# Kernel optimization log

Hardware: AMD Instinct MI355X
Metric: run time of the kernel (lower is better)

The kernel has to match this reference:

```python
import jax, jax.numpy as jnp
import numpy as np
import math

EMB, HEADS, LATENT, FFN = 1024, 16, 256, 4096
HEAD_DIM = EMB // HEADS
B, N = 2, 2048
EPS = 1e-5


def _layer_norm(x, g, b):
    m = jnp.mean(x, axis=-1, keepdims=True)
    v = jnp.mean(jnp.square(x - m), axis=-1, keepdims=True)
    return (x - m) * jax.lax.rsqrt(v + EPS) * g + b


def setup_inputs() -> dict:
    key = jax.random.key(0)
    ks = jax.random.split(key, 20)
    s = 0.02
    def w(k, shape):
        return jax.random.normal(k, shape, dtype=jnp.float32) * s
    return {
        "x": jax.random.normal(ks[0], (B, N, EMB), dtype=jnp.float32),
        "attn_bias": jax.random.normal(ks[1], (N, N), dtype=jnp.float32),
        "Wq_w": w(ks[2], (EMB, EMB)),   "Wq_b": jnp.zeros((EMB,), jnp.float32),
        "WaK_w": w(ks[3], (EMB, LATENT)), "WaK_b": jnp.zeros((LATENT,), jnp.float32),
        "WbK_w": w(ks[4], (LATENT, EMB)), "WbK_b": jnp.zeros((EMB,), jnp.float32),
        "WaV_w": w(ks[5], (EMB, LATENT)), "WaV_b": jnp.zeros((LATENT,), jnp.float32),
        "WbV_w": w(ks[6], (LATENT, EMB)), "WbV_b": jnp.zeros((EMB,), jnp.float32),
        "Wo_w": w(ks[7], (EMB, EMB)),   "Wo_b": jnp.zeros((EMB,), jnp.float32),
        "ffn1_w": w(ks[8], (EMB, FFN)), "ffn1_b": jnp.zeros((FFN,), jnp.float32),
        "ffn2_w": w(ks[9], (FFN, EMB)), "ffn2_b": jnp.zeros((EMB,), jnp.float32),
        "ln1_g": jnp.ones((EMB,), jnp.float32), "ln1_b": jnp.zeros((EMB,), jnp.float32),
        "ln2_g": jnp.ones((EMB,), jnp.float32), "ln2_b": jnp.zeros((EMB,), jnp.float32),
    }


def reference(x, attn_bias, Wq_w, Wq_b, WaK_w, WaK_b, WbK_w, WbK_b,
              WaV_w, WaV_b, WbV_w, WbV_b, Wo_w, Wo_b,
              ffn1_w, ffn1_b, ffn2_w, ffn2_b, ln1_g, ln1_b, ln2_g, ln2_b):
    b, n, _ = x.shape
    Q = x @ Wq_w + Wq_b                                   # [B,N,E]
    K = (x @ WaK_w + WaK_b) @ WbK_w + WbK_b               # low-rank K
    V = (x @ WaV_w + WaV_b) @ WbV_w + WbV_b               # low-rank V
    Qh = Q.reshape(b, n, HEADS, HEAD_DIM)
    Kh = K.reshape(b, n, HEADS, HEAD_DIM)
    Vh = V.reshape(b, n, HEADS, HEAD_DIM)
    scale = 1.0 / math.sqrt(HEAD_DIM)
    scores = jnp.einsum('bnhd,bmhd->bhnm', Qh, Kh) * scale
    scores = scores + attn_bias[None, None, :, :]
    weights = jax.nn.softmax(scores, axis=-1)
    O = jnp.einsum('bhnm,bmhd->bnhd', weights, Vh).reshape(b, n, EMB)
    O = O @ Wo_w + Wo_b
    x1 = _layer_norm(x + O, ln1_g, ln1_b)
    h = jax.nn.gelu(x1 @ ffn1_w + ffn1_b, approximate=False)
    ffn_out = h @ ffn2_w + ffn2_b
    return _layer_norm(x1 + ffn_out, ln2_g, ln2_b)
```

## Files before the change

kernel.cpp:

```cpp
#include <hip/hip_runtime.h>
#include <hip/hip_bf16.h>
#include <math.h>

typedef __attribute__((ext_vector_type(4))) float f32x4;
typedef __attribute__((ext_vector_type(8))) __bf16 bf16x8;
typedef unsigned short u16;

#define L2E 1.44269504088896f

__device__ __forceinline__ u16 f2b(float f) {
  union { float f; unsigned u; } x; x.f = f;
  unsigned r = x.u + 0x7fffu + ((x.u >> 16) & 1u);
  return (u16)(r >> 16);
}

__device__ __forceinline__ void gl_lds16(const void* g, void* l) {
  __builtin_amdgcn_global_load_lds(
      (const __attribute__((address_space(1))) void*)g,
      (__attribute__((address_space(3))) void*)l, 16, 0, 0);
}

template<int EPI>
__global__ __launch_bounds__(256, 3)
void gemm_bt(const u16* __restrict__ A, int lda,
             const u16* __restrict__ Bt,
             const float* __restrict__ bias,
             void* __restrict__ C, int ldc,
             int M, int N, int K)
{
  __shared__ u16 As[128 * 32];
  __shared__ u16 Bs[128 * 32];
  const int t = threadIdx.x;
  const int lane = t & 63;
  const int w = t >> 6;
  const int wr = w >> 1, wc = w & 1;
  const int row0 = blockIdx.y * 128, col0 = blockIdx.x * 128;
  const int r = lane & 15, g = lane >> 4;

  f32x4 acc[4][4];
#pragma unroll
  for (int m = 0; m < 4; ++m)
#pragma unroll
    for (int n = 0; n < 4; ++n) acc[m][n] = (f32x4){0.f, 0.f, 0.f, 0.f};

  const u16* Ag = A + (size_t)(row0 + (t >> 2)) * lda + (t & 3) * 8;
  const u16* Bg = Bt + (size_t)(col0 + (t >> 2)) * K + (t & 3) * 8;
  u16* Asw  = &As[t * 8];
  u16* Asw2 = &As[(t + 256) * 8];
  u16* Bsw  = &Bs[t * 8];
  u16* Bsw2 = &Bs[(t + 256) * 8];
  const size_t a2 = (size_t)64 * lda, bo2 = (size_t)64 * K;

  for (int kt = 0; kt < K; kt += 32) {
    gl_lds16(Ag + kt, Asw);
    gl_lds16(Ag + a2 + kt, Asw2);
    gl_lds16(Bg + kt, Bsw);
    gl_lds16(Bg + bo2 + kt, Bsw2);
    __syncthreads();
    bf16x8 af[4], bfr[4];
#pragma unroll
    for (int m = 0; m < 4; ++m)
      af[m] = *(const bf16x8*)&As[(wr * 64 + m * 16 + r) * 32 + g * 8];
#pragma unroll
    for (int n = 0; n < 4; ++n)
      bfr[n] = *(const bf16x8*)&Bs[(wc * 64 + n * 16 + r) * 32 + g * 8];
#pragma unroll
    for (int m = 0; m < 4; ++m)
#pragma unroll
      for (int n = 0; n < 4; ++n)
        acc[m][n] = __builtin_amdgcn_mfma_f32_16x16x32_bf16(af[m], bfr[n], acc[m][n], 0, 0, 0);
    __syncthreads();
  }

#pragma unroll
  for (int n = 0; n < 4; ++n) {
    const int col = col0 + wc * 64 + n * 16 + r;
    const float bv = bias[col];
#pragma unroll
    for (int m = 0; m < 4; ++m) {
      const int rb = row0 + wr * 64 + m * 16 + g * 4;
      if constexpr (EPI == 3) {
        const int b_ = rb >> 11, nn = rb & 2047;
        const int h_ = col >> 6, d_ = col & 63;
        u16* vp = (u16*)C + ((size_t)((b_ * 16 + h_) * 64 + d_)) * 2048 + nn;
        ushort4 pk;
        pk.x = f2b(acc[m][n][0] + bv);
        pk.y = f2b(acc[m][n][1] + bv);
        pk.z = f2b(acc[m][n][2] + bv);
        pk.w = f2b(acc[m][n][3] + bv);
        *(ushort4*)vp = pk;
      } else {
#pragma unroll
        for (int j = 0; j < 4; ++j) {
          float v = acc[m][n][j] + bv;
          if constexpr (EPI == 1) v = 0.5f * v * (1.0f + erff(v * 0.70710678118654752f));
          const size_t idx = (size_t)(rb + j) * ldc + col;
          if constexpr (EPI == 2) ((float*)C)[idx] = v;
          else ((u16*)C)[idx] = f2b(v);
        }
      }
    }
  }
}

__global__ __launch_bounds__(256, 4)
void attn_kernel(const u16* __restrict__ Qg,
                 const u16* __restrict__ Kg,
                 const u16* __restrict__ Vt,
                 const float* __restrict__ Bf,
                 u16* __restrict__ O)
{
  const int bh = blockIdx.x;
  const int b = bh >> 4, h = bh & 15;
  const int q0 = blockIdx.y * 64;
  const int t = threadIdx.x;
  const int lane = t & 63;
  const int w = t >> 6;
  const int r = lane & 15, g = lane >> 4;

  __shared__ u16 Ks[64 * 64];
  __shared__ u16 Vs[64 * 64];
  __shared__ __bf16 Ps[4][16 * 64];

  bf16x8 qa[2];
  {
    const size_t qrow = (size_t)(b * 2048 + q0 + w * 16 + r);
    const u16* qp = Qg + qrow * 1536 + h * 64 + g * 8;
    qa[0] = *(const bf16x8*)qp;
    qa[1] = *(const bf16x8*)(qp + 32);
#pragma unroll
    for (int dh = 0; dh < 2; ++dh)
#pragma unroll
      for (int i = 0; i < 8; ++i)
        qa[dh][i] = (__bf16)((float)qa[dh][i] * (0.125f * L2E));
  }

  f32x4 Oa[4];
#pragma unroll
  for (int dc = 0; dc < 4; ++dc) Oa[dc] = (f32x4){0.f, 0.f, 0.f, 0.f};
  float lsum[4] = {0.f, 0.f, 0.f, 0.f};

  const int srow = t >> 3;
  const int spos = t & 7;
  const int sseg  = spos ^ (srow & 7);
  const int srow2 = srow + 32;
  const int sseg2 = spos ^ (srow2 & 7);

  const float* bp = Bf + (size_t)(q0 + w * 16 + g * 4) * 2048 + r;

  for (int mt = 0; mt < 32; ++mt) {
    const int m0 = mt * 64;
    gl_lds16(Kg + (size_t)(b * 2048 + m0 + srow)  * 1024 + h * 64 + sseg * 8,  &Ks[t * 8]);
    gl_lds16(Kg + (size_t)(b * 2048 + m0 + srow2) * 1024 + h * 64 + sseg2 * 8, &Ks[(t + 256) * 8]);
    gl_lds16(Vt + (size_t)(bh * 64 + srow)  * 2048 + m0 + sseg * 8,  &Vs[t * 8]);
    gl_lds16(Vt + (size_t)(bh * 64 + srow2) * 2048 + m0 + sseg2 * 8, &Vs[(t + 256) * 8]);

    f32x4 s[4];
#pragma unroll
    for (int mc = 0; mc < 4; ++mc)
#pragma unroll
      for (int j = 0; j < 4; ++j)
        s[mc][j] = bp[(size_t)j * 2048 + m0 + mc * 16] * L2E;

    __syncthreads();

#pragma unroll
    for (int mc = 0; mc < 4; ++mc) {
      const int mrow = mc * 16 + r;
      const bf16x8 kb0 = *(const bf16x8*)&Ks[mrow * 64 + (((0 * 4 + g) ^ (mrow & 7)) * 8)];
      const bf16x8 kb1 = *(const bf16x8*)&Ks[mrow * 64 + (((1 * 4 + g) ^ (mrow & 7)) * 8)];
      s[mc] = __builtin_amdgcn_mfma_f32_16x16x32_bf16(qa[0], kb0, s[mc], 0, 0, 0);
      s[mc] = __builtin_amdgcn_mfma_f32_16x16x32_bf16(qa[1], kb1, s[mc], 0, 0, 0);
    }

    __bf16* pw = (__bf16*)Ps[w];
#pragma unroll
    for (int mc = 0; mc < 4; ++mc) {
      const int mm = mc * 16 + r;
#pragma unroll
      for (int j = 0; j < 4; ++j) {
        const float p = __builtin_amdgcn_exp2f(s[mc][j]);
        lsum[j] += p;
        const int qr = g * 4 + j;
        pw[qr * 64 + (((mm >> 3) ^ (qr & 7)) * 8) + (mm & 7)] = (__bf16)p;
      }
    }

    const bf16x8 pa0 = *(const bf16x8*)&pw[r * 64 + (((0 * 4 + g) ^ (r & 7)) * 8)];
    const bf16x8 pa1 = *(const bf16x8*)&pw[r * 64 + (((1 * 4 + g) ^ (r & 7)) * 8)];
#pragma unroll
    for (int dc = 0; dc < 4; ++dc) {
      const int drow = dc * 16 + r;
      const bf16x8 vb0 = *(const bf16x8*)&Vs[drow * 64 + (((0 * 4 + g) ^ (drow & 7)) * 8)];
      const bf16x8 vb1 = *(const bf16x8*)&Vs[drow * 64 + (((1 * 4 + g) ^ (drow & 7)) * 8)];
      Oa[dc] = __builtin_amdgcn_mfma_f32_16x16x32_bf16(pa0, vb0, Oa[dc], 0, 0, 0);
      Oa[dc] = __builtin_amdgcn_mfma_f32_16x16x32_bf16(pa1, vb1, Oa[dc], 0, 0, 0);
    }
    __syncthreads();
  }

#pragma unroll
  for (int off = 1; off < 16; off <<= 1)
#pragma unroll
    for (int j = 0; j < 4; ++j) lsum[j] += __shfl_xor(lsum[j], off);

  u16* Os = Ks;
#pragma unroll
  for (int j = 0; j < 4; ++j) {
    const float inv = 1.0f / lsum[j];
    const int qr = w * 16 + g * 4 + j;
#pragma unroll
    for (int dc = 0; dc < 4; ++dc)
      Os[qr * 64 + dc * 16 + r] = f2b(Oa[dc][j] * inv);
  }
  __syncthreads();
#pragma unroll
  for (int i = 0; i < 2; ++i) {
    const int tt = t + i * 256;
    const int orow = tt >> 3, oseg = tt & 7;
    const uint4 v = *(const uint4*)&Os[orow * 64 + oseg * 8];
    *(uint4*)&O[(size_t)(b * 2048 + q0 + orow) * 1024 + h * 64 + oseg * 8] = v;
  }
}

__global__ void cvt_f32_bf16(const float* __restrict__ in, u16* __restrict__ out, int n4)
{
  const int i = blockIdx.x * 256 + threadIdx.x;
  if (i >= n4) return;
  const float4 v = ((const float4*)in)[i];
  ushort4 o;
  o.x = f2b(v.x); o.y = f2b(v.y); o.z = f2b(v.z); o.w = f2b(v.w);
  ((ushort4*)out)[i] = o;
}

__global__ __launch_bounds__(256)
void transpose_f32_bf16(const float* __restrict__ in, u16* __restrict__ out, int R, int C)
{
  __shared__ float tile[32][33];
  const int tx = threadIdx.x, ty = threadIdx.y;
  const int c0 = blockIdx.x * 32, r0 = blockIdx.y * 32;
#pragma unroll
  for (int i = 0; i < 4; ++i)
    tile[ty + i * 8][tx] = in[(size_t)(r0 + ty + i * 8) * C + c0 + tx];
  __syncthreads();
#pragma unroll
  for (int i = 0; i < 4; ++i)
    out[(size_t)(c0 + ty + i * 8) * R + r0 + tx] = f2b(tile[tx][ty + i * 8]);
}

__global__ void concat_bias(const float* __restrict__ a, const float* __restrict__ b,
                            const float* __restrict__ c, float* __restrict__ o)
{
  const int i = blockIdx.x * 256 + threadIdx.x;
  if (i < 1024) o[i] = a[i];
  else if (i < 1280) o[i] = b[i - 1024];
  else if (i < 1536) o[i] = c[i - 1280];
}

template<int WB>
__global__ __launch_bounds__(256)
void ln_kernel(const float* __restrict__ xa, const float* __restrict__ xbr,
               const float* __restrict__ gam, const float* __restrict__ bet,
               float* __restrict__ outf, u16* __restrict__ outb)
{
  const int row = blockIdx.x, t = threadIdx.x;
  const float4 a = ((const float4*)(xa + (size_t)row * 1024))[t];
  const float4 c = ((const float4*)(xbr + (size_t)row * 1024))[t];
  const float v0 = a.x + c.x, v1 = a.y + c.y, v2 = a.z + c.z, v3 = a.w + c.w;
  float s = v0 + v1 + v2 + v3;
  float q = v0 * v0 + v1 * v1 + v2 * v2 + v3 * v3;
#pragma unroll
  for (int off = 1; off < 64; off <<= 1) {
    s += __shfl_xor(s, off);
    q += __shfl_xor(q, off);
  }
  __shared__ float ss[4], qs[4];
  const int w = t >> 6, lane = t & 63;
  if (lane == 0) { ss[w] = s; qs[w] = q; }
  __syncthreads();
  const float S = ss[0] + ss[1] + ss[2] + ss[3];
  const float Q = qs[0] + qs[1] + qs[2] + qs[3];
  const float mean = S * (1.0f / 1024.0f);
  const float var = Q * (1.0f / 1024.0f) - mean * mean;
  const float rstd = rsqrtf(var + 1e-5f);
  const float4 gm = ((const float4*)gam)[t];
  const float4 bt = ((const float4*)bet)[t];
  const float o0 = (v0 - mean) * rstd * gm.x + bt.x;
  const float o1 = (v1 - mean) * rstd * gm.y + bt.y;
  const float o2 = (v2 - mean) * rstd * gm.z + bt.z;
  const float o3 = (v3 - mean) * rstd * gm.w + bt.w;
  float4 ov; ov.x = o0; ov.y = o1; ov.z = o2; ov.w = o3;
  ((float4*)(outf + (size_t)row * 1024))[t] = ov;
  if constexpr (WB) {
    ushort4 ob; ob.x = f2b(o0); ob.y = f2b(o1); ob.z = f2b(o2); ob.w = f2b(o3);
    ((ushort4*)(outb + (size_t)row * 1024))[t] = ob;
  }
}

extern "C" void kernel_launch(void* const* d_in, const int* in_sizes, int n_in,
                              void* d_out, int out_size, void* d_ws, size_t ws_size,
                              hipStream_t stream)
{
  const float* x     = (const float*)d_in[0];
  const float* abias = (const float*)d_in[1];
  const float* Wq_w  = (const float*)d_in[2];
  const float* Wq_b  = (const float*)d_in[3];
  const float* WaK_w = (const float*)d_in[4];
  const float* WaK_b = (const float*)d_in[5];
  const float* WbK_w = (const float*)d_in[6];
  const float* WbK_b = (const float*)d_in[7];
  const float* WaV_w = (const float*)d_in[8];
  const float* WaV_b = (const float*)d_in[9];
  const float* WbV_w = (const float*)d_in[10];
  const float* WbV_b = (const float*)d_in[11];
  const float* Wo_w  = (const float*)d_in[12];
  const float* Wo_b  = (const float*)d_in[13];
  const float* f1_w  = (const float*)d_in[14];
  const float* f1_b  = (const float*)d_in[15];
  const float* f2_w  = (const float*)d_in[16];
  const float* f2_b  = (const float*)d_in[17];
  const float* ln1_g = (const float*)d_in[18];
  const float* ln1_b = (const float*)d_in[19];
  const float* ln2_g = (const float*)d_in[20];
  const float* ln2_b = (const float*)d_in[21];

  char* ws = (char*)d_ws;
  u16*   xb    = (u16*)(ws + 0);
  u16*   WB1   = (u16*)(ws + 8388608);
  u16*   WbKT  = (u16*)(ws + 11534336);
  u16*   WbVT  = (u16*)(ws + 12058624);
  u16*   WoT   = (u16*)(ws + 12582912);
  u16*   F1T   = (u16*)(ws + 14680064);
  u16*   F2T   = (u16*)(ws + 23068672);
  float* bias1 = (float*)(ws + 31457280);
  u16*   G1    = (u16*)(ws + 39854080);
  u16*   Kb    = (u16*)(ws + 52436992);
  u16*   Vt    = (u16*)(ws + 60825600);
  u16*   Ob    = (u16*)(ws + 69214208);
  float* Y     = (float*)(ws + 77602816);
  float* x1f   = (float*)(ws + 94380032);
  u16*   x1b   = (u16*)(ws + 111157248);
  u16*   hbuf  = G1;

  cvt_f32_bf16<<<4096, 256, 0, stream>>>(x, xb, 1048576);
  transpose_f32_bf16<<<dim3(32, 32), dim3(32, 8), 0, stream>>>(Wq_w, WB1, 1024, 1024);
  transpose_f32_bf16<<<dim3(8, 32),  dim3(32, 8), 0, stream>>>(WaK_w, WB1 + 1024 * 1024, 1024, 256);
  transpose_f32_bf16<<<dim3(8, 32),  dim3(32, 8), 0, stream>>>(WaV_w, WB1 + 1280 * 1024, 1024, 256);
  transpose_f32_bf16<<<dim3(32, 8),  dim3(32, 8), 0, stream>>>(WbK_w, WbKT, 256, 1024);
  transpose_f32_bf16<<<dim3(32, 8),  dim3(32, 8), 0, stream>>>(WbV_w, WbVT, 256, 1024);
  transpose_f32_bf16<<<dim3(32, 32), dim3(32, 8), 0, stream>>>(Wo_w, WoT, 1024, 1024);
  transpose_f32_bf16<<<dim3(128, 32), dim3(32, 8), 0, stream>>>(f1_w, F1T, 1024, 4096);
  transpose_f32_bf16<<<dim3(32, 128), dim3(32, 8), 0, stream>>>(f2_w, F2T, 4096, 1024);
  concat_bias<<<6, 256, 0, stream>>>(Wq_b, WaK_b, WaV_b, bias1);

  gemm_bt<0><<<dim3(12, 32), 256, 0, stream>>>(xb, 1024, WB1, bias1, G1, 1536, 4096, 1536, 1024);
  gemm_bt<0><<<dim3(8, 32), 256, 0, stream>>>(G1 + 1024, 1536, WbKT, WbK_b, Kb, 1024, 4096, 1024, 256);
  gemm_bt<3><<<dim3(8, 32), 256, 0, stream>>>(G1 + 1280, 1536, WbVT, WbV_b, Vt, 2048, 4096, 1024, 256);
  attn_kernel<<<dim3(32, 32), 256, 0, stream>>>(G1, Kb, Vt, abias, Ob);
  gemm_bt<2><<<dim3(8, 32), 256, 0, stream>>>(Ob, 1024, WoT, Wo_b, Y, 1024, 4096, 1024, 1024);
  ln_kernel<1><<<4096, 256, 0, stream>>>(x, Y, ln1_g, ln1_b, x1f, x1b);
  gemm_bt<1><<<dim3(32, 32), 256, 0, stream>>>(x1b, 1024, F1T, f1_b, hbuf, 4096, 4096, 4096, 1024);
  gemm_bt<2><<<dim3(8, 32), 256, 0, stream>>>(hbuf, 4096, F2T, f2_b, Y, 1024, 4096, 1024, 4096);
  ln_kernel<0><<<4096, 256, 0, stream>>>(x1f, Y, ln2_g, ln2_b, (float*)d_out, nullptr);
}
```

Before: 471.7 us.

## Add split-K for FFN2, narrower tiles for N=1024 GEMMs, fuse weight transposes

Templates the GEMM on column-tile width and split-K factor. The N=1024 GEMMs now use 64-wide tiles, doubling block count for better CU occupancy. FFN2 is split into two K halves writing separate fp32 partials, which the final LayerNorm sums. The eight weight transpose launches are merged into one kernel to cut launch overhead. Costs are extra partial-buffer traffic and a reused workspace region for the second partial.

```diff
diff --git a/kernel.cpp b/kernel.cpp
--- a/kernel.cpp
+++ b/kernel.cpp
@@ -20,62 +20,72 @@
       (__attribute__((address_space(3))) void*)l, 16, 0, 0);
 }
 
-template<int EPI>
+template<int EPI, int BN, int SPLITK>
 __global__ __launch_bounds__(256, 3)
 void gemm_bt(const u16* __restrict__ A, int lda,
              const u16* __restrict__ Bt,
              const float* __restrict__ bias,
-             void* __restrict__ C, int ldc,
+             void* __restrict__ C, void* __restrict__ C2, int ldc,
              int M, int N, int K)
 {
+  constexpr int NF = BN / 32;
   __shared__ u16 As[128 * 32];
-  __shared__ u16 Bs[128 * 32];
+  __shared__ u16 Bs[BN * 32];
   const int t = threadIdx.x;
   const int lane = t & 63;
   const int w = t >> 6;
   const int wr = w >> 1, wc = w & 1;
-  const int row0 = blockIdx.y * 128, col0 = blockIdx.x * 128;
+  const int row0 = blockIdx.y * 128, col0 = blockIdx.x * BN;
   const int r = lane & 15, g = lane >> 4;
 
-  f32x4 acc[4][4];
+  f32x4 acc[4][NF];
 #pragma unroll
   for (int m = 0; m < 4; ++m)
 #pragma unroll
-    for (int n = 0; n < 4; ++n) acc[m][n] = (f32x4){0.f, 0.f, 0.f, 0.f};
-
-  const u16* Ag = A + (size_t)(row0 + (t >> 2)) * lda + (t & 3) * 8;
-  const u16* Bg = Bt + (size_t)(col0 + (t >> 2)) * K + (t & 3) * 8;
+    for (int n = 0; n < NF; ++n) acc[m][n] = (f32x4){0.f, 0.f, 0.f, 0.f};
+
+  const int KS = K / SPLITK;
+  const int kbeg = (SPLITK > 1) ? blockIdx.z * KS : 0;
+
+  const u16* Ag = A + (size_t)(row0 + (t >> 2)) * lda + (t & 3) * 8 + kbeg;
+  const u16* Bg = Bt + (size_t)(col0 + (t >> 2)) * K + (t & 3) * 8 + kbeg;
   u16* Asw  = &As[t * 8];
   u16* Asw2 = &As[(t + 256) * 8];
   u16* Bsw  = &Bs[t * 8];
-  u16* Bsw2 = &Bs[(t + 256) * 8];
+  u16* Bsw2 = (BN == 128) ? &Bs[(t + 256) * 8] : nullptr;
   const size_t a2 = (size_t)64 * lda, bo2 = (size_t)64 * K;
 
-  for (int kt = 0; kt < K; kt += 32) {
+  for (int kt = 0; kt < KS; kt += 32) {
     gl_lds16(Ag + kt, Asw);
     gl_lds16(Ag + a2 + kt, Asw2);
     gl_lds16(Bg + kt, Bsw);
-    gl_lds16(Bg + bo2 + kt, Bsw2);
+    if constexpr (BN == 128) gl_lds16(Bg + bo2 + kt, Bsw2);
     __syncthreads();
-    bf16x8 af[4], bfr[4];
+    bf16x8 af[4], bfr[NF];
 #pragma unroll
     for (int m = 0; m < 4; ++m)
       af[m] = *(const bf16x8*)&As[(wr * 64 + m * 16 + r) * 32 + g * 8];
 #pragma unroll
-    for (int n = 0; n < 4; ++n)
-      bfr[n] = *(const bf16x8*)&Bs[(wc * 64 + n * 16 + r) * 32 + g * 8];
+    for (int n = 0; n < NF; ++n)
+      bfr[n] = *(const bf16x8*)&Bs[(wc * (BN / 2) + n * 16 + r) * 32 + g * 8];
 #pragma unroll
     for (int m = 0; m < 4; ++m)
 #pragma unroll
-      for (int n = 0; n < 4; ++n)
+      for (int n = 0; n < NF; ++n)
         acc[m][n] = __builtin_amdgcn_mfma_f32_16x16x32_bf16(af[m], bfr[n], acc[m][n], 0, 0, 0);
     __syncthreads();
   }
 
-#pragma unroll
-  for (int n = 0; n < 4; ++n) {
-    const int col = col0 + wc * 64 + n * 16 + r;
-    const float bv = bias[col];
+  bool addb = true;
+  float* Cf = (float*)C;
+  if constexpr (SPLITK > 1) {
+    if (blockIdx.z != 0) { addb = false; Cf = (float*)C2; }
+  }
+
+#pragma unroll
+  for (int n = 0; n < NF; ++n) {
+    const int col = col0 + wc * (BN / 2) + n * 16 + r;
+    const float bv = addb ? bias[col] : 0.f;
 #pragma unroll
     for (int m = 0; m < 4; ++m) {
       const int rb = row0 + wr * 64 + m * 16 + g * 4;
@@ -95,7 +105,7 @@
           float v = acc[m][n][j] + bv;
           if constexpr (EPI == 1) v = 0.5f * v * (1.0f + erff(v * 0.70710678118654752f));
           const size_t idx = (size_t)(rb + j) * ldc + col;
-          if constexpr (EPI == 2) ((float*)C)[idx] = v;
+          if constexpr (EPI == 2) Cf[idx] = v;
           else ((u16*)C)[idx] = f2b(v);
         }
       }
@@ -223,6 +233,39 @@
   }
 }
 
+__global__ __launch_bounds__(256)
+void prep_weights(const float* __restrict__ Wq, const float* __restrict__ WaK,
+                  const float* __restrict__ WaV, const float* __restrict__ WbK,
+                  const float* __restrict__ WbV, const float* __restrict__ Wo,
+                  const float* __restrict__ F1, const float* __restrict__ F2,
+                  u16* __restrict__ WB1, u16* __restrict__ WbKT,
+                  u16* __restrict__ WbVT, u16* __restrict__ WoT,
+                  u16* __restrict__ F1T, u16* __restrict__ F2T)
+{
+  const int bid = blockIdx.x;
+  const float* src; u16* dst; int R, C, tile, tilesX;
+  if (bid < 1024)      { src = Wq;  dst = WB1;             R = 1024; C = 1024; tile = bid;        tilesX = 32; }
+  else if (bid < 1280) { src = WaK; dst = WB1 + 1024*1024; R = 1024; C = 256;  tile = bid - 1024; tilesX = 8; }
+  else if (bid < 1536) { src = WaV; dst = WB1 + 1280*1024; R = 1024; C = 256;  tile = bid - 1280; tilesX = 8; }
+  else if (bid < 1792) { src = WbK; dst = WbKT;            R = 256;  C = 1024; tile = bid - 1536; tilesX = 32; }
+  else if (bid < 2048) { src = WbV; dst = WbVT;            R = 256;  C = 1024; tile = bid - 1792; tilesX = 32; }
+  else if (bid < 3072) { src = Wo;  dst = WoT;             R = 1024; C = 1024; tile = bid - 2048; tilesX = 32; }
+  else if (bid < 7168) { src = F1;  dst = F1T;             R = 1024; C = 4096; tile = bid - 3072; tilesX = 128; }
+  else                 { src = F2;  dst = F2T;             R = 4096; C = 1024; tile = bid - 7168; tilesX = 32; }
+  const int bx = tile % tilesX, by = tile / tilesX;
+  const int c0 = bx * 32, r0 = by * 32;
+
+  __shared__ float tl[32][33];
+  const int tx = threadIdx.x, ty = threadIdx.y;
+#pragma unroll
+  for (int i = 0; i < 4; ++i)
+    tl[ty + i * 8][tx] = src[(size_t)(r0 + ty + i * 8) * C + c0 + tx];
+  __syncthreads();
+#pragma unroll
+  for (int i = 0; i < 4; ++i)
+    dst[(size_t)(c0 + ty + i * 8) * R + r0 + tx] = f2b(tl[tx][ty + i * 8]);
+}
+
 __global__ void cvt_f32_bf16(const float* __restrict__ in, u16* __restrict__ out, int n4)
 {
   const int i = blockIdx.x * 256 + threadIdx.x;
@@ -233,21 +276,6 @@
   ((ushort4*)out)[i] = o;
 }
 
-__global__ __launch_bounds__(256)
-void transpose_f32_bf16(const float* __restrict__ in, u16* __restrict__ out, int R, int C)
-{
-  __shared__ float tile[32][33];
-  const int tx = threadIdx.x, ty = threadIdx.y;
-  const int c0 = blockIdx.x * 32, r0 = blockIdx.y * 32;
-#pragma unroll
-  for (int i = 0; i < 4; ++i)
-    tile[ty + i * 8][tx] = in[(size_t)(r0 + ty + i * 8) * C + c0 + tx];
-  __syncthreads();
-#pragma unroll
-  for (int i = 0; i < 4; ++i)
-    out[(size_t)(c0 + ty + i * 8) * R + r0 + tx] = f2b(tile[tx][ty + i * 8]);
-}
-
 __global__ void concat_bias(const float* __restrict__ a, const float* __restrict__ b,
                             const float* __restrict__ c, float* __restrict__ o)
 {
@@ -257,16 +285,21 @@
   else if (i < 1536) o[i] = c[i - 1280];
 }
 
-template<int WB>
+template<int WB, int NP>
 __global__ __launch_bounds__(256)
-void ln_kernel(const float* __restrict__ xa, const float* __restrict__ xbr,
+void ln_kernel(const float* __restrict__ xa, const float* __restrict__ y0,
+               const float* __restrict__ y1,
                const float* __restrict__ gam, const float* __restrict__ bet,
                float* __restrict__ outf, u16* __restrict__ outb)
 {
   const int row = blockIdx.x, t = threadIdx.x;
   const float4 a = ((const float4*)(xa + (size_t)row * 1024))[t];
-  const float4 c = ((const float4*)(xbr + (size_t)row * 1024))[t];
-  const float v0 = a.x + c.x, v1 = a.y + c.y, v2 = a.z + c.z, v3 = a.w + c.w;
+  const float4 c = ((const float4*)(y0 + (size_t)row * 1024))[t];
+  float v0 = a.x + c.x, v1 = a.y + c.y, v2 = a.z + c.z, v3 = a.w + c.w;
+  if constexpr (NP == 2) {
+    const float4 d = ((const float4*)(y1 + (size_t)row * 1024))[t];
+    v0 += d.x; v1 += d.y; v2 += d.z; v3 += d.w;
+  }
   float s = v0 + v1 + v2 + v3;
   float q = v0 * v0 + v1 * v1 + v2 * v2 + v3 * v3;
 #pragma unroll
@@ -341,25 +374,21 @@
   float* x1f   = (float*)(ws + 94380032);
   u16*   x1b   = (u16*)(ws + 111157248);
   u16*   hbuf  = G1;
-
+  float* Y1    = (float*)(ws + 0);
+
+  prep_weights<<<11264, dim3(32, 8), 0, stream>>>(Wq_w, WaK_w, WaV_w, WbK_w, WbV_w,
+                                                  Wo_w, f1_w, f2_w,
+                                                  WB1, WbKT, WbVT, WoT, F1T, F2T);
   cvt_f32_bf16<<<4096, 256, 0, stream>>>(x, xb, 1048576);
-  transpose_f32_bf16<<<dim3(32, 32), dim3(32, 8), 0, stream>>>(Wq_w, WB1, 1024, 1024);
-  transpose_f32_bf16<<<dim3(8, 32),  dim3(32, 8), 0, stream>>>(WaK_w, WB1 + 1024 * 1024, 1024, 256);
-  transpose_f32_bf16<<<dim3(8, 32),  dim3(32, 8), 0, stream>>>(WaV_w, WB1 + 1280 * 1024, 1024, 256);
-  transpose_f32_bf16<<<dim3(32, 8),  dim3(32, 8), 0, stream>>>(WbK_w, WbKT, 256, 1024);
-  transpose_f32_bf16<<<dim3(32, 8),  dim3(32, 8), 0, stream>>>(WbV_w, WbVT, 256, 1024);
-  transpose_f32_bf16<<<dim3(32, 32), dim3(32, 8), 0, stream>>>(Wo_w, WoT, 1024, 1024);
-  transpose_f32_bf16<<<dim3(128, 32), dim3(32, 8), 0, stream>>>(f1_w, F1T, 1024, 4096);
-  transpose_f32_bf16<<<dim3(32, 128), dim3(32, 8), 0, stream>>>(f2_w, F2T, 4096, 1024);
   concat_bias<<<6, 256, 0, stream>>>(Wq_b, WaK_b, WaV_b, bias1);
 
-  gemm_bt<0><<<dim3(12, 32), 256, 0, stream>>>(xb, 1024, WB1, bias1, G1, 1536, 4096, 1536, 1024);
-  gemm_bt<0><<<dim3(8, 32), 256, 0, stream>>>(G1 + 1024, 1536, WbKT, WbK_b, Kb, 1024, 4096, 1024, 256);
-  gemm_bt<3><<<dim3(8, 32), 256, 0, stream>>>(G1 + 1280, 1536, WbVT, WbV_b, Vt, 2048, 4096, 1024, 256);
+  gemm_bt<0, 128, 1><<<dim3(12, 32), 256, 0, stream>>>(xb, 1024, WB1, bias1, G1, nullptr, 1536, 4096, 1536, 1024);
+  gemm_bt<0, 64, 1><<<dim3(16, 32), 256, 0, stream>>>(G1 + 1024, 1536, WbKT, WbK_b, Kb, nullptr, 1024, 4096, 1024, 256);
+  gemm_bt<3, 64, 1><<<dim3(16, 32), 256, 0, stream>>>(G1 + 1280, 1536, WbVT, WbV_b, Vt, nullptr, 2048, 4096, 1024, 256);
   attn_kernel<<<dim3(32, 32), 256, 0, stream>>>(G1, Kb, Vt, abias, Ob);
-  gemm_bt<2><<<dim3(8, 32), 256, 0, stream>>>(Ob, 1024, WoT, Wo_b, Y, 1024, 4096, 1024, 1024);
-  ln_kernel<1><<<4096, 256, 0, stream>>>(x, Y, ln1_g, ln1_b, x1f, x1b);
-  gemm_bt<1><<<dim3(32, 32), 256, 0, stream>>>(x1b, 1024, F1T, f1_b, hbuf, 4096, 4096, 4096, 1024);
-  gemm_bt<2><<<dim3(8, 32), 256, 0, stream>>>(hbuf, 4096, F2T, f2_b, Y, 1024, 4096, 1024, 4096);
-  ln_kernel<0><<<4096, 256, 0, stream>>>(x1f, Y, ln2_g, ln2_b, (float*)d_out, nullptr);
-}
+  gemm_bt<2, 64, 1><<<dim3(16, 32), 256, 0, stream>>>(Ob, 1024, WoT, Wo_b, Y, nullptr, 1024, 4096, 1024, 1024);
+  ln_kernel<1, 1><<<4096, 256, 0, stream>>>(x, Y, Y, ln1_g, ln1_b, x1f, x1b);
+  gemm_bt<1, 128, 1><<<dim3(32, 32), 256, 0, stream>>>(x1b, 1024, F1T, f1_b, hbuf, nullptr, 4096, 4096, 4096, 1024);
+  gemm_bt<2, 128, 2><<<dim3(8, 32, 2), 256, 0, stream>>>(hbuf, 4096, F2T, f2_b, Y, Y1, 1024, 4096, 1024, 4096);
+  ln_kernel<0, 2><<<4096, 256, 0, stream>>>(x1f, Y, Y1, ln2_g, ln2_b, (float*)d_out, nullptr);
+}
```

Measured after the change: 417.7 us. 1.13x faster.
